# Optimization experiments

Measured on AMD Instinct MI355X. Metric: run time of the kernel, lower is better.

## Reference

```python
import jax, jax.numpy as jnp
import numpy as np

B = 65536  # batch size


def setup_inputs() -> dict:
    key = jax.random.key(0)
    kx, kw, kb = jax.random.split(key, 3)
    x = jax.random.normal(kx, (B, 784), dtype=jnp.float32)
    W = jax.random.normal(kw, (10, 784), dtype=jnp.float32) * 0.03
    b = jax.random.normal(kb, (10,), dtype=jnp.float32) * 0.03
    return {"x": x, "W": W, "b": b}


def _quanv_features(x):
    # x: [B, 784] -> [B, 28, 28] -> 2x2 patches in row-major patch order,
    # each patch flattened as [p(r,c), p(r,c+1), p(r+1,c), p(r+1,c+1)].
    Bn = x.shape[0]
    p = x.reshape(Bn, 14, 2, 14, 2).transpose(0, 1, 3, 2, 4).reshape(Bn, 196, 4)
    # Analytic 4-qubit circuit: RY(x_i)|0>, CNOT(0,1), CNOT(2,3), <Z_i>
    # => [cos x0, cos x0 * cos x1, cos x2, cos x2 * cos x3]
    c = jnp.cos(p)
    m = jnp.stack(
        [c[..., 0], c[..., 0] * c[..., 1], c[..., 2], c[..., 2] * c[..., 3]],
        axis=-1,
    )
    # residual add with the raw patch, then concat over 196 patches -> [B, 784]
    return (m + p).reshape(Bn, 784)


def reference(x, W, b):
    feats = _quanv_features(x)              # [B, 784]
    logits = feats @ W.T + b                # [B, 10]
    return jax.nn.log_softmax(logits, axis=-1)
```

## Files before the change

kernel.cpp:

```cpp
#include <hip/hip_runtime.h>
#include <hip/hip_bf16.h>
#include <stdint.h>


typedef __attribute__((ext_vector_type(8))) short short8;
typedef __attribute__((ext_vector_type(4))) float f32x4;

__device__ __forceinline__ short bf16h(float g) {
    return (short)((__float_as_uint(g) + 0x8000u) >> 16);
}

__global__ void quanv_wprep_kernel(const float* __restrict__ Wm,
                                   uint32_t* __restrict__ ws) {
    const int idx = blockIdx.x * 256 + threadIdx.x;
    if (idx >= 6400) return;
    const int kt  = idx >> 8;
    const int rem = idx & 255;
    const int l   = rem >> 2;
    const int d   = rem & 3;
    const int n   = l & 15;
    const int kg  = l >> 4;
    uint32_t outv = 0;
    if (n < 10) {
        uint32_t hv[2];
#pragma unroll
        for (int d2 = 0; d2 < 2; ++d2) {
            const int e  = 2 * d + d2;
            const int jp = 32 * kt + 4 * kg + 16 * (e >> 2) + 2 * ((e >> 1) & 1);
            float v = 0.f;
            if (jp < 784) {
                const int ri = jp / 28;
                const int pc = (jp % 28) >> 1;
                const int pr = ri >> 1;
                const int ho = ri & 1;
                const int col = (pr * 14 + pc) * 4 + 2 * ho + (e & 1);
                v = Wm[n * 784 + col];
            }
            hv[d2] = (uint32_t)__bfloat16_as_ushort(__float2bfloat16(v));
        }
        outv = hv[0] | (hv[1] << 16);
    }
    ws[idx] = outv;
}

#define FEAT8(VA, VB, A) do {                                                 \
    { const float ce=__cosf((VA)[0]), co=__cosf((VA)[1]);                     \
      (A)[0] = bf16h(ce + (VA)[0]);                                           \
      (A)[1] = bf16h(fmaf(ce, co, (VA)[1])); }                                \
    { const float ce=__cosf((VA)[2]), co=__cosf((VA)[3]);                     \
      (A)[2] = bf16h(ce + (VA)[2]);                                           \
      (A)[3] = bf16h(fmaf(ce, co, (VA)[3])); }                                \
    { const float ce=__cosf((VB)[0]), co=__cosf((VB)[1]);                     \
      (A)[4] = bf16h(ce + (VB)[0]);                                           \
      (A)[5] = bf16h(fmaf(ce, co, (VB)[1])); }                                \
    { const float ce=__cosf((VB)[2]), co=__cosf((VB)[3]);                     \
      (A)[6] = bf16h(ce + (VB)[2]);                                           \
      (A)[7] = bf16h(fmaf(ce, co, (VB)[3])); }                                \
} while (0)

template <int KT0, int N>
__device__ __forceinline__ void quarter(const float* __restrict__ px,
                                        const char* __restrict__ wsb,
                                        int l, f32x4& acc) {
    f32x4 va[N], vb[N];
    short8 wf[N];
    const char* wbp = wsb + KT0 * 1024 + l * 16;
#pragma unroll
    for (int j = 0; j < N; ++j) {
        const int kt = KT0 + j;
        va[j] = *(const f32x4*)(px + 32 * kt);
        vb[j] = (kt == 24) ? *(const f32x4*)(px)
                           : *(const f32x4*)(px + 32 * kt + 16);
        wf[j] = *(const short8*)(wbp + j * 1024);
    }
#pragma unroll
    for (int j = 0; j < N; ++j) {
        short8 a;
        FEAT8(va[j], vb[j], a);
        acc = __builtin_amdgcn_mfma_f32_16x16x32_bf16(a, wf[j], acc, 0, 0, 0);
    }
}

__global__ __launch_bounds__(256, 4)
void quanv_mfma11_kernel(const float* __restrict__ x,
                         const char* __restrict__ wsb,
                         const float* __restrict__ bias,
                         float* __restrict__ out) {
    __shared__ float red[4][16][16];

    const int t   = threadIdx.x;
    const int l   = t & 63;
    const int kq  = __builtin_amdgcn_readfirstlane(t >> 6);
    const int r16 = l & 15;
    const int kg  = l >> 4;
    const int rowBase = blockIdx.x * 16;
    const float* px = x + (size_t)(rowBase + r16) * 784 + 4 * kg;

    f32x4 acc = {0.f, 0.f, 0.f, 0.f};

    if      (kq == 0) quarter<0, 7>(px, wsb, l, acc);
    else if (kq == 1) quarter<7, 6>(px, wsb, l, acc);
    else if (kq == 2) quarter<13, 6>(px, wsb, l, acc);
    else              quarter<19, 6>(px, wsb, l, acc);

#pragma unroll
    for (int j = 0; j < 4; ++j) red[kq][4 * kg + j][r16] = acc[j];
    __syncthreads();

    if (t < 16) {
        const int r = t;
        float lg[10];
#pragma unroll
        for (int n = 0; n < 10; ++n)
            lg[n] = red[0][r][n] + red[1][r][n] + red[2][r][n] + red[3][r][n]
                  + bias[n];

        float mx = lg[0];
#pragma unroll
        for (int n = 1; n < 10; ++n) mx = fmaxf(mx, lg[n]);
        float sum = 0.f;
#pragma unroll
        for (int n = 0; n < 10; ++n) sum += __expf(lg[n] - mx);
        const float ls = __logf(sum) + mx;

        float* o = out + (size_t)(rowBase + r) * 10;
#pragma unroll
        for (int n = 0; n < 10; n += 2)
            *(float2*)(o + n) = make_float2(lg[n] - ls, lg[n + 1] - ls);
    }
}

extern "C" void kernel_launch(void* const* d_in, const int* in_sizes, int n_in,
                              void* d_out, int out_size, void* d_ws, size_t ws_size,
                              hipStream_t stream) {
    const float* x    = (const float*)d_in[0];
    const float* Wm   = (const float*)d_in[1];
    const float* bias = (const float*)d_in[2];
    float* out        = (float*)d_out;

    quanv_wprep_kernel<<<dim3(25), dim3(256), 0, stream>>>(
        Wm, (uint32_t*)d_ws);
    quanv_mfma11_kernel<<<dim3(4096), dim3(256), 0, stream>>>(
        x, (const char*)d_ws, bias, out);
}
```

Before: 39.16 us.

## Stage input row tile into LDS via direct global-to-LDS loads

Each block now copies its 16 contiguous input rows into shared memory with global_load_lds 16-byte transfers, then reads the patch values from LDS for the feature and MFMA computation. This replaces strided per-lane global vector loads with fully coalesced contiguous copies. It adds a large LDS allocation that lowers occupancy, plus an extra barrier that serialises the load and compute phases within a block.

```diff
diff --git a/kernel.cpp b/kernel.cpp
--- a/kernel.cpp
+++ b/kernel.cpp
@@ -5,6 +5,13 @@
 
 typedef __attribute__((ext_vector_type(8))) short short8;
 typedef __attribute__((ext_vector_type(4))) float f32x4;
+
+typedef __attribute__((address_space(1))) const void GAS;
+typedef __attribute__((address_space(3))) void LAS;
+
+__device__ __forceinline__ void gl_lds16(const void* g, void* l) {
+    __builtin_amdgcn_global_load_lds((GAS*)g, (LAS*)l, 16, 0, 0);
+}
 
 __device__ __forceinline__ short bf16h(float g) {
     return (short)((__float_as_uint(g) + 0x8000u) >> 16);
@@ -59,34 +66,31 @@
 } while (0)
 
 template <int KT0, int N>
-__device__ __forceinline__ void quarter(const float* __restrict__ px,
-                                        const char* __restrict__ wsb,
-                                        int l, f32x4& acc) {
-    f32x4 va[N], vb[N];
+__device__ __forceinline__ void quarter_lds(const char* __restrict__ lb,
+                                            const char* __restrict__ wbp0,
+                                            f32x4& acc) {
     short8 wf[N];
-    const char* wbp = wsb + KT0 * 1024 + l * 16;
+#pragma unroll
+    for (int j = 0; j < N; ++j)
+        wf[j] = *(const short8*)(wbp0 + (KT0 + j) * 1024);
 #pragma unroll
     for (int j = 0; j < N; ++j) {
         const int kt = KT0 + j;
-        va[j] = *(const f32x4*)(px + 32 * kt);
-        vb[j] = (kt == 24) ? *(const f32x4*)(px)
-                           : *(const f32x4*)(px + 32 * kt + 16);
-        wf[j] = *(const short8*)(wbp + j * 1024);
-    }
-#pragma unroll
-    for (int j = 0; j < N; ++j) {
+        const f32x4 va = *(const f32x4*)(lb + 128 * kt);
+        const f32x4 vb = (kt == 24) ? *(const f32x4*)(lb)
+                                    : *(const f32x4*)(lb + 128 * kt + 64);
         short8 a;
-        FEAT8(va[j], vb[j], a);
+        FEAT8(va, vb, a);
         acc = __builtin_amdgcn_mfma_f32_16x16x32_bf16(a, wf[j], acc, 0, 0, 0);
     }
 }
 
-__global__ __launch_bounds__(256, 4)
-void quanv_mfma11_kernel(const float* __restrict__ x,
+__global__ __launch_bounds__(256, 3)
+void quanv_mfma12_kernel(const float* __restrict__ x,
                          const char* __restrict__ wsb,
                          const float* __restrict__ bias,
                          float* __restrict__ out) {
-    __shared__ float red[4][16][16];
+    __shared__ char smraw[50176];
 
     const int t   = threadIdx.x;
     const int l   = t & 63;
@@ -94,17 +98,31 @@
     const int r16 = l & 15;
     const int kg  = l >> 4;
     const int rowBase = blockIdx.x * 16;
-    const float* px = x + (size_t)(rowBase + r16) * 784 + 4 * kg;
+    const char* gtile = (const char*)x + (size_t)rowBase * 3136;
 
+    const int c0 = (kq == 0) ? 0 : 13 + (kq - 1) * 12;
+    const int nc = (kq == 0) ? 13 : 12;
+    for (int j = 0; j < nc; ++j) {
+        const int c = c0 + j;
+        const uint32_t lof = __builtin_amdgcn_readfirstlane((uint32_t)(c * 1024));
+        gl_lds16(gtile + c * 1024 + l * 16, smraw + lof);
+    }
+    __syncthreads();
+
+    const char* lb   = smraw + r16 * 3136 + 16 * kg;
+    const char* wbp0 = wsb + l * 16;
     f32x4 acc = {0.f, 0.f, 0.f, 0.f};
+    if      (kq == 0) quarter_lds<0, 7>(lb, wbp0, acc);
+    else if (kq == 1) quarter_lds<7, 6>(lb, wbp0, acc);
+    else if (kq == 2) quarter_lds<13, 6>(lb, wbp0, acc);
+    else              quarter_lds<19, 6>(lb, wbp0, acc);
 
-    if      (kq == 0) quarter<0, 7>(px, wsb, l, acc);
-    else if (kq == 1) quarter<7, 6>(px, wsb, l, acc);
-    else if (kq == 2) quarter<13, 6>(px, wsb, l, acc);
-    else              quarter<19, 6>(px, wsb, l, acc);
+    __syncthreads();
 
+    float* red = (float*)smraw;
 #pragma unroll
-    for (int j = 0; j < 4; ++j) red[kq][4 * kg + j][r16] = acc[j];
+    for (int j = 0; j < 4; ++j)
+        red[(kq * 16 + 4 * kg + j) * 16 + r16] = acc[j];
     __syncthreads();
 
     if (t < 16) {
@@ -112,7 +130,8 @@
         float lg[10];
 #pragma unroll
         for (int n = 0; n < 10; ++n)
-            lg[n] = red[0][r][n] + red[1][r][n] + red[2][r][n] + red[3][r][n]
+            lg[n] = red[(0 * 16 + r) * 16 + n] + red[(1 * 16 + r) * 16 + n]
+                  + red[(2 * 16 + r) * 16 + n] + red[(3 * 16 + r) * 16 + n]
                   + bias[n];
 
         float mx = lg[0];
@@ -140,6 +159,6 @@
 
     quanv_wprep_kernel<<<dim3(25), dim3(256), 0, stream>>>(
         Wm, (uint32_t*)d_ws);
-    quanv_mfma11_kernel<<<dim3(4096), dim3(256), 0, stream>>>(
+    quanv_mfma12_kernel<<<dim3(4096), dim3(256), 0, stream>>>(
         x, (const char*)d_ws, bias, out);
 }
```

Measured after the change: 41.41 us. 5.7% more time.
